# Optimization experiments

Hardware: AMD Instinct MI355X
Metric: run time of the kernel (lower is better)

## Reference

```python
import jax, jax.numpy as jnp
import numpy as np

B, CIN, G, H, HW, WMIX = 128, 64, 8, 14, 16, 16  # batch, in-ch, groups, spatial, mixed width


def setup_inputs() -> dict:
    key = jax.random.key(0)
    k1, k2, k3 = jax.random.split(key, 3)
    x = jax.random.normal(k1, (B, CIN, G, H, H), dtype=jnp.float32)
    w_conv = jax.random.normal(k2, (G, 3, 3, 32), dtype=jnp.float32)   # weights[0]
    w_mix = jax.random.normal(k3, (CIN, WMIX), dtype=jnp.float32)       # weights[1]
    return {"x": x, "w_conv": w_conv, "w_mix": w_mix}


def _unfold3(t, axis, size):
    # torch F.unfold with kernel (3,1), padding (1,0) along `axis`: zero-pad by 1
    # and stack the 3 shifted windows as a new axis inserted at `axis`.
    pad = [(0, 0)] * t.ndim
    pad[axis] = (1, 1)
    p = jnp.pad(t, pad)
    slices = []
    for k in range(3):
        idx = [slice(None)] * t.ndim
        idx[axis] = slice(k, k + size)
        slices.append(p[tuple(idx)])
    return jnp.stack(slices, axis=axis)


def reference(x, w_conv, w_mix):
    # channel mix: (B, 64, 8, 14, 14) x (64, 16) -> (B, 8, 14, 14, 16)
    t4 = jnp.einsum('kjmnl,ji->kmnli', x, w_mix)
    # first unfold along H (axis 3): (B, 8, 14, 3, 14, 16)
    u1 = _unfold3(t4, 3, H)
    # second unfold along H (now axis 4): (B, 8, 14, 3, 3, 14, 16)
    u2 = _unfold3(u1, 4, H)
    # permute (0,1,2,5,4,3,6) -> (B, 8, 14, 14, 3, 3, 16)
    t5 = jnp.transpose(u2, (0, 1, 2, 5, 4, 3, 6))
    # conv channel mix: contract group(8) and both 3-taps -> (B, 14, 14, 16, 32)
    t6 = jnp.einsum('mlonikp,likj->monpj', t5, w_conv)
    # (B, 14, 14, 32, 16) -> (B, 14, 14, 512)
    t7 = jnp.transpose(t6, (0, 1, 2, 4, 3)).reshape(B, H, H, 512)
    t7 = jnp.roll(t7, 1, axis=1)  # shift_direction fixed to +1
    return jnp.transpose(t7, (0, 3, 1, 2))  # (B, 512, 14, 14)
```

## Files before the change

kernel.cpp:

```cpp
#include <hip/hip_runtime.h>

static constexpr int NB   = 128;
static constexpr int NCIN = 64;
static constexpr int NG   = 8;
static constexpr int NH   = 14;
static constexpr int NP   = 16;
static constexpr int HH   = NH * NH;
static constexpr int LROW = 20;

static constexpr int OFF_T4 = 0;
static constexpr int OFF_W2 = 2560;
static constexpr int OFF_WC = 3840;
static constexpr int LDS_FLOATS = 4352;

#define FMAQ(buf, qb)                                                          \
    do {                                                                       \
        _Pragma("unroll")                                                      \
        for (int j4 = 0; j4 < 4; j4++) {                                       \
            _Pragma("unroll")                                                  \
            for (int pp = 0; pp < 8; pp++) {                                   \
                const int p_ = p0 + pp;            \
                am[pp] += buf[j4 * 4 + 0] * wmix[((qb) + j4 * 4 + 0) * NP + p_]\
                        + buf[j4 * 4 + 1] * wmix[((qb) + j4 * 4 + 1) * NP + p_]\
                        + buf[j4 * 4 + 2] * wmix[((qb) + j4 * 4 + 2) * NP + p_]\
                        + buf[j4 * 4 + 3] * wmix[((qb) + j4 * 4 + 3) * NP + p_];\
            }                                                                  \
        }                                                                      \
    } while (0)

__global__ __launch_bounds__(256, 8) void fused_kernel(const float* __restrict__ x,
                                                       const float* __restrict__ wconv,
                                                       const float* __restrict__ wmix,
                                                       float* __restrict__ out) {
    __shared__ __align__(16) float lds[LDS_FLOATS];
    float* t4s = lds + OFF_T4;
    float* w2s = lds + OFF_W2;
    float* wcs = lds + OFF_WC;

    const int tid = threadIdx.x;
    const int bid = blockIdx.x;
    const int xcd = bid & 7;
    const int t8  = bid >> 3;
    const int o   = t8 % NH;
    const int b   = xcd + 8 * (t8 / NH);
    const int o_src = (o + NH - 1) % NH;

    const int gW = tid >> 5, jW = tid & 31;
    float wv9[9];
    {
        const float* wp = wconv + (size_t)(gW * 9) * 32 + jW;
#pragma unroll
        for (int t = 0; t < 9; t++) wv9[t] = wp[t * 32];
    }

    const int  lane128 = tid & 127;
    const bool xact    = lane128 < 112;
    const int  gS      = lane128 / 14;
    const int  lS      = lane128 % 14;
    const int  p0      = __builtin_amdgcn_readfirstlane((tid >> 7) << 3);
    const float* xg    = x + (size_t)b * (NCIN * NG * HH) + (size_t)gS * HH
                           + o_src * NH + lS;

    float xq0[16], xq1[16];
    if (xact) {
#pragma unroll
        for (int r = 0; r < 16; r++) xq0[r] = xg[(size_t)r * (NG * HH)];
    }

    {
        float d0 = wv9[0];
        float d1 = wv9[1] + wv9[3];
        float d2 = wv9[2] + wv9[4] + wv9[6];
        float d3 = wv9[5] + wv9[7];
        float d4 = wv9[8];
        float* wp2 = w2s + gW * 160 + jW;
        wp2[0]   = d0;
        wp2[32]  = d1;
        wp2[64]  = d2;
        wp2[96]  = d3;
        wp2[128] = d4;
        wcs[gW * 32 + jW]       = wv9[2];
        wcs[256 + gW * 32 + jW] = wv9[6];
    }
#pragma unroll
    for (int r = 0; r < 3; r++) {
        int idx = r * 256 + tid;
        int gp  = idx / 6;
        int s   = idx % 6;
        int l2  = (s < 2) ? s : (14 + s);
        t4s[gp * LROW + l2] = 0.f;
    }

    float am[8] = {0.f, 0.f, 0.f, 0.f, 0.f, 0.f, 0.f, 0.f};
    if (xact) {
#pragma unroll
        for (int r = 0; r < 16; r++) xq1[r] = xg[(size_t)(16 + r) * (NG * HH)];
        FMAQ(xq0, 0);
#pragma unroll
        for (int r = 0; r < 16; r++) xq0[r] = xg[(size_t)(32 + r) * (NG * HH)];
        FMAQ(xq1, 16);
#pragma unroll
        for (int r = 0; r < 16; r++) xq1[r] = xg[(size_t)(48 + r) * (NG * HH)];
        FMAQ(xq0, 32);
        FMAQ(xq1, 48);
#pragma unroll
        for (int pp = 0; pp < 8; pp++) {
            t4s[(gS * 16 + p0 + pp) * LROW + lS + 2] = am[pp];
        }
    }
    __syncthreads();

    const int p  = tid & 15;
    const int jh = tid >> 4;
    const int jb = jh * 2;

    float acc[NH][2];
#pragma unroll
    for (int n = 0; n < NH; n++) { acc[n][0] = 0.f; acc[n][1] = 0.f; }

    for (int g = 0; g < NG; g++) {
        float row[LROW];
        const float* rp = &t4s[(g * 16 + p) * LROW];
#pragma unroll
        for (int q = 0; q < 5; q++) {
            float4 v = *reinterpret_cast<const float4*>(rp + q * 4);
            row[q * 4 + 0] = v.x; row[q * 4 + 1] = v.y;
            row[q * 4 + 2] = v.z; row[q * 4 + 3] = v.w;
        }
#pragma unroll
        for (int di = 0; di < 5; di++) {
            float2 w = *reinterpret_cast<const float2*>(&w2s[(g * 5 + di) * 32 + jb]);
#pragma unroll
            for (int n = 0; n < NH; n++) {
                float rv = row[n + di];
                acc[n][0] += rv * w.x;
                acc[n][1] += rv * w.y;
            }
        }
        float2 c0 = *reinterpret_cast<const float2*>(&wcs[g * 32 + jb]);
        float2 c1 = *reinterpret_cast<const float2*>(&wcs[256 + g * 32 + jb]);
        float r2 = row[2], r15 = row[15];
        acc[0][0]  -= r2  * c0.x; acc[0][1]  -= r2  * c0.y;
        acc[13][0] -= r15 * c1.x; acc[13][1] -= r15 * c1.y;
    }

    __syncthreads();

    int rotw = jh * 2;
    rotw -= (rotw >= 14) ? 14 : 0;
    rotw -= (rotw >= 14) ? 14 : 0;

    const int k7 = tid & 7;
    const int cb = tid >> 3;
    float* ob = out + (size_t)b * 512 * HH + (size_t)o * NH;

#pragma unroll
    for (int h = 0; h < 2; h++) {
        if ((jh >> 3) == h) {
#pragma unroll
            for (int jj = 0; jj < 2; jj++) {
                int cl = ((jb + jj) * 16 + p) & 255;
                int sb = cl * 15;
#pragma unroll
                for (int n = 0; n < NH; n++) {
                    int rn = n + rotw;
                    rn -= (rn >= 14) ? 14 : 0;
                    lds[sb + rn] = acc[n][jj];
                }
            }
        }
        __syncthreads();
        if (k7 < 7) {
#pragma unroll
            for (int r = 0; r < 8; r++) {
                int cl  = cb + 32 * r;
                int cg  = h * 256 + cl;
                int rot = (2 * (h * 8 + r)) % 14;
                int rn  = 2 * k7 + rot;
                rn -= (rn >= 14) ? 14 : 0;
                float v0 = lds[cl * 15 + rn];
                float v1 = lds[cl * 15 + rn + 1];
                *reinterpret_cast<float2*>(ob + (size_t)cg * HH + 2 * k7) =
                    make_float2(v0, v1);
            }
        }
        __syncthreads();
    }
}

extern "C" void kernel_launch(void* const* d_in, const int* in_sizes, int n_in,
                              void* d_out, int out_size, void* d_ws, size_t ws_size,
                              hipStream_t stream) {
    const float* x     = (const float*)d_in[0];
    const float* wconv = (const float*)d_in[1];
    const float* wmix  = (const float*)d_in[2];
    float* out = (float*)d_out;
    (void)d_ws; (void)ws_size;

    fused_kernel<<<NB * NH, 256, 0, stream>>>(x, wconv, wmix, out);
}
```

Before: 133.8 us.

## Process two output rows per block and overlap second mix with first conv

Each block now handles two consecutive output rows, which halves the grid and amortises the weight loads and LDS weight setup. The channel-mix global loads for the second row are issued before the first row's convolution, and a separate LDS staging region lets the first row's store run while the second row's input sits in LDS. In exchange, LDS use per block nearly doubles, launch bounds drop to 4 blocks per CU, and register pressure rises because mix results are held across the conv phase.

```diff
diff --git a/kernel.cpp b/kernel.cpp
--- a/kernel.cpp
+++ b/kernel.cpp
@@ -11,7 +11,8 @@
 static constexpr int OFF_T4 = 0;
 static constexpr int OFF_W2 = 2560;
 static constexpr int OFF_WC = 3840;
-static constexpr int LDS_FLOATS = 4352;
+static constexpr int OFF_ST = 4352;
+static constexpr int LDS_FLOATS = 8192;
 
 #define FMAQ(buf, qb)                                                          \
     do {                                                                       \
@@ -28,7 +29,104 @@
         }                                                                      \
     } while (0)
 
-__global__ __launch_bounds__(256, 8) void fused_kernel(const float* __restrict__ x,
+__device__ __forceinline__ void mix_tile(const float* __restrict__ xg,
+                                         const float* __restrict__ wmix,
+                                         int p0, bool xact, float am[8]) {
+#pragma unroll
+    for (int pp = 0; pp < 8; pp++) am[pp] = 0.f;
+    if (!xact) return;
+    float xq0[16], xq1[16];
+#pragma unroll
+    for (int r = 0; r < 16; r++) xq0[r] = xg[(size_t)r * (NG * HH)];
+#pragma unroll
+    for (int r = 0; r < 16; r++) xq1[r] = xg[(size_t)(16 + r) * (NG * HH)];
+    FMAQ(xq0, 0);
+#pragma unroll
+    for (int r = 0; r < 16; r++) xq0[r] = xg[(size_t)(32 + r) * (NG * HH)];
+    FMAQ(xq1, 16);
+#pragma unroll
+    for (int r = 0; r < 16; r++) xq1[r] = xg[(size_t)(48 + r) * (NG * HH)];
+    FMAQ(xq0, 32);
+    FMAQ(xq1, 48);
+}
+
+__device__ __forceinline__ void conv_tile(const float* __restrict__ t4s,
+                                          const float* __restrict__ w2s,
+                                          const float* __restrict__ wcs,
+                                          int p, int jb, float acc[NH][2]) {
+#pragma unroll
+    for (int n = 0; n < NH; n++) { acc[n][0] = 0.f; acc[n][1] = 0.f; }
+    for (int g = 0; g < NG; g++) {
+        float row[LROW];
+        const float* rp = &t4s[(g * 16 + p) * LROW];
+#pragma unroll
+        for (int q = 0; q < 5; q++) {
+            float4 v = *reinterpret_cast<const float4*>(rp + q * 4);
+            row[q * 4 + 0] = v.x; row[q * 4 + 1] = v.y;
+            row[q * 4 + 2] = v.z; row[q * 4 + 3] = v.w;
+        }
+#pragma unroll
+        for (int di = 0; di < 5; di++) {
+            float2 w = *reinterpret_cast<const float2*>(&w2s[(g * 5 + di) * 32 + jb]);
+#pragma unroll
+            for (int n = 0; n < NH; n++) {
+                float rv = row[n + di];
+                acc[n][0] += rv * w.x;
+                acc[n][1] += rv * w.y;
+            }
+        }
+        float2 c0 = *reinterpret_cast<const float2*>(&wcs[g * 32 + jb]);
+        float2 c1 = *reinterpret_cast<const float2*>(&wcs[256 + g * 32 + jb]);
+        float r2 = row[2], r15 = row[15];
+        acc[0][0]  -= r2  * c0.x; acc[0][1]  -= r2  * c0.y;
+        acc[13][0] -= r15 * c1.x; acc[13][1] -= r15 * c1.y;
+    }
+}
+
+__device__ __forceinline__ void stage_store(float* __restrict__ stg,
+                                            float* __restrict__ ob,
+                                            int tid, int p, int jh, int jb,
+                                            const float acc[NH][2]) {
+    int rotw = jh * 2;
+    rotw -= (rotw >= 14) ? 14 : 0;
+    rotw -= (rotw >= 14) ? 14 : 0;
+    const int k7 = tid & 7;
+    const int cb = tid >> 3;
+#pragma unroll
+    for (int h = 0; h < 2; h++) {
+        if ((jh >> 3) == h) {
+#pragma unroll
+            for (int jj = 0; jj < 2; jj++) {
+                int cl = ((jb + jj) * 16 + p) & 255;
+                int sb = cl * 15;
+#pragma unroll
+                for (int n = 0; n < NH; n++) {
+                    int rn = n + rotw;
+                    rn -= (rn >= 14) ? 14 : 0;
+                    stg[sb + rn] = acc[n][jj];
+                }
+            }
+        }
+        __syncthreads();
+        if (k7 < 7) {
+#pragma unroll
+            for (int r = 0; r < 8; r++) {
+                int cl  = cb + 32 * r;
+                int cg  = h * 256 + cl;
+                int rot = (2 * (h * 8 + r)) % 14;
+                int rn  = 2 * k7 + rot;
+                rn -= (rn >= 14) ? 14 : 0;
+                float v0 = stg[cl * 15 + rn];
+                float v1 = stg[cl * 15 + rn + 1];
+                *reinterpret_cast<float2*>(ob + (size_t)cg * HH + 2 * k7) =
+                    make_float2(v0, v1);
+            }
+        }
+        __syncthreads();
+    }
+}
+
+__global__ __launch_bounds__(256, 4) void fused_kernel(const float* __restrict__ x,
                                                        const float* __restrict__ wconv,
                                                        const float* __restrict__ wmix,
                                                        float* __restrict__ out) {
@@ -36,14 +134,18 @@
     float* t4s = lds + OFF_T4;
     float* w2s = lds + OFF_W2;
     float* wcs = lds + OFF_WC;
+    float* stg = lds + OFF_ST;
 
     const int tid = threadIdx.x;
     const int bid = blockIdx.x;
     const int xcd = bid & 7;
     const int t8  = bid >> 3;
-    const int o   = t8 % NH;
-    const int b   = xcd + 8 * (t8 / NH);
-    const int o_src = (o + NH - 1) % NH;
+    const int q   = t8 % 7;
+    const int b   = xcd + 8 * (t8 / 7);
+    const int o0  = 2 * q;
+    const int o1  = 2 * q + 1;
+    const int os0 = (o0 + NH - 1) % NH;
+    const int os1 = o0;
 
     const int gW = tid >> 5, jW = tid & 31;
     float wv9[9];
@@ -58,14 +160,7 @@
     const int  gS      = lane128 / 14;
     const int  lS      = lane128 % 14;
     const int  p0      = __builtin_amdgcn_readfirstlane((tid >> 7) << 3);
-    const float* xg    = x + (size_t)b * (NCIN * NG * HH) + (size_t)gS * HH
-                           + o_src * NH + lS;
-
-    float xq0[16], xq1[16];
-    if (xact) {
-#pragma unroll
-        for (int r = 0; r < 16; r++) xq0[r] = xg[(size_t)r * (NG * HH)];
-    }
+    const float* xgb   = x + (size_t)b * (NCIN * NG * HH) + (size_t)gS * HH + lS;
 
     {
         float d0 = wv9[0];
@@ -91,101 +186,34 @@
         t4s[gp * LROW + l2] = 0.f;
     }
 
-    float am[8] = {0.f, 0.f, 0.f, 0.f, 0.f, 0.f, 0.f, 0.f};
+    float am[8];
+    mix_tile(xgb + os0 * NH, wmix, p0, xact, am);
     if (xact) {
 #pragma unroll
-        for (int r = 0; r < 16; r++) xq1[r] = xg[(size_t)(16 + r) * (NG * HH)];
-        FMAQ(xq0, 0);
-#pragma unroll
-        for (int r = 0; r < 16; r++) xq0[r] = xg[(size_t)(32 + r) * (NG * HH)];
-        FMAQ(xq1, 16);
-#pragma unroll
-        for (int r = 0; r < 16; r++) xq1[r] = xg[(size_t)(48 + r) * (NG * HH)];
-        FMAQ(xq0, 32);
-        FMAQ(xq1, 48);
-#pragma unroll
-        for (int pp = 0; pp < 8; pp++) {
+        for (int pp = 0; pp < 8; pp++)
             t4s[(gS * 16 + p0 + pp) * LROW + lS + 2] = am[pp];
-        }
     }
     __syncthreads();
+
+    mix_tile(xgb + os1 * NH, wmix, p0, xact, am);
 
     const int p  = tid & 15;
     const int jh = tid >> 4;
     const int jb = jh * 2;
-
     float acc[NH][2];
-#pragma unroll
-    for (int n = 0; n < NH; n++) { acc[n][0] = 0.f; acc[n][1] = 0.f; }
-
-    for (int g = 0; g < NG; g++) {
-        float row[LROW];
-        const float* rp = &t4s[(g * 16 + p) * LROW];
-#pragma unroll
-        for (int q = 0; q < 5; q++) {
-            float4 v = *reinterpret_cast<const float4*>(rp + q * 4);
-            row[q * 4 + 0] = v.x; row[q * 4 + 1] = v.y;
-            row[q * 4 + 2] = v.z; row[q * 4 + 3] = v.w;
-        }
-#pragma unroll
-        for (int di = 0; di < 5; di++) {
-            float2 w = *reinterpret_cast<const float2*>(&w2s[(g * 5 + di) * 32 + jb]);
-#pragma unroll
-            for (int n = 0; n < NH; n++) {
-                float rv = row[n + di];
-                acc[n][0] += rv * w.x;
-                acc[n][1] += rv * w.y;
-            }
-        }
-        float2 c0 = *reinterpret_cast<const float2*>(&wcs[g * 32 + jb]);
-        float2 c1 = *reinterpret_cast<const float2*>(&wcs[256 + g * 32 + jb]);
-        float r2 = row[2], r15 = row[15];
-        acc[0][0]  -= r2  * c0.x; acc[0][1]  -= r2  * c0.y;
-        acc[13][0] -= r15 * c1.x; acc[13][1] -= r15 * c1.y;
-    }
-
+    conv_tile(t4s, w2s, wcs, p, jb, acc);
     __syncthreads();
 
-    int rotw = jh * 2;
-    rotw -= (rotw >= 14) ? 14 : 0;
-    rotw -= (rotw >= 14) ? 14 : 0;
-
-    const int k7 = tid & 7;
-    const int cb = tid >> 3;
-    float* ob = out + (size_t)b * 512 * HH + (size_t)o * NH;
-
-#pragma unroll
-    for (int h = 0; h < 2; h++) {
-        if ((jh >> 3) == h) {
-#pragma unroll
-            for (int jj = 0; jj < 2; jj++) {
-                int cl = ((jb + jj) * 16 + p) & 255;
-                int sb = cl * 15;
-#pragma unroll
-                for (int n = 0; n < NH; n++) {
-                    int rn = n + rotw;
-                    rn -= (rn >= 14) ? 14 : 0;
-                    lds[sb + rn] = acc[n][jj];
-                }
-            }
-        }
-        __syncthreads();
-        if (k7 < 7) {
-#pragma unroll
-            for (int r = 0; r < 8; r++) {
-                int cl  = cb + 32 * r;
-                int cg  = h * 256 + cl;
-                int rot = (2 * (h * 8 + r)) % 14;
-                int rn  = 2 * k7 + rot;
-                rn -= (rn >= 14) ? 14 : 0;
-                float v0 = lds[cl * 15 + rn];
-                float v1 = lds[cl * 15 + rn + 1];
-                *reinterpret_cast<float2*>(ob + (size_t)cg * HH + 2 * k7) =
-                    make_float2(v0, v1);
-            }
-        }
-        __syncthreads();
-    }
+    if (xact) {
+#pragma unroll
+        for (int pp = 0; pp < 8; pp++)
+            t4s[(gS * 16 + p0 + pp) * LROW + lS + 2] = am[pp];
+    }
+    float* obase = out + (size_t)b * 512 * HH;
+    stage_store(stg, obase + (size_t)o0 * NH, tid, p, jh, jb, acc);
+
+    conv_tile(t4s, w2s, wcs, p, jb, acc);
+    stage_store(stg, obase + (size_t)o1 * NH, tid, p, jh, jb, acc);
 }
 
 extern "C" void kernel_launch(void* const* d_in, const int* in_sizes, int n_in,
@@ -197,5 +225,5 @@
     float* out = (float*)d_out;
     (void)d_ws; (void)ws_size;
 
-    fused_kernel<<<NB * NH, 256, 0, stream>>>(x, wconv, wmix, out);
-}
+    fused_kernel<<<NB * NH / 2, 256, 0, stream>>>(x, wconv, wmix, out);
+}
```

New measurement: 204.9 us. 53.1% more time.
